# Performance work log

Measured on AMD Instinct MI355X. Metric: run time of the kernel, lower is better.

Reference implementation:

```python
import jax, jax.numpy as jnp
import numpy as np

MEMORY_SIZE = 40
INPUT_SIZE = 256
OUTPUT_SIZE = 256
BATCH = 16
SEQ = 4096


def setup_inputs() -> dict:
    key = jax.random.key(0)
    k1, k2, k3, k4 = jax.random.split(key, 4)
    x = jax.random.normal(k1, (BATCH, SEQ, INPUT_SIZE), dtype=jnp.float32)
    # xavier-uniform-style init for params
    lim_w = float(np.sqrt(6.0 / (INPUT_SIZE + OUTPUT_SIZE)))
    W1 = jax.random.uniform(k2, (INPUT_SIZE, OUTPUT_SIZE), minval=-lim_w, maxval=lim_w, dtype=jnp.float32)
    W2 = jax.random.uniform(k3, (INPUT_SIZE, OUTPUT_SIZE), minval=-lim_w, maxval=lim_w, dtype=jnp.float32)
    bias = jnp.ones((OUTPUT_SIZE,), dtype=jnp.float32)
    lim_m = float(np.sqrt(6.0 / (MEMORY_SIZE + 1 + INPUT_SIZE)))
    mw = jax.random.uniform(k4, (MEMORY_SIZE + 1, INPUT_SIZE), minval=-lim_m, maxval=lim_m, dtype=jnp.float32)
    mw = mw.at[0].set(0.0)  # torch init zeros row 0 (it stays trainable though)
    return {"input_data": x, "W1": W1, "W2": W2, "bias": bias, "memory_weights": mw}


def reference(input_data, W1, W2, bias, memory_weights):
    # Faithful to: idx(i,j) = i-j if 1 <= i-j <= memory_size else 0;
    # h_hatt[b,i,d] = sum_j memory_weights[idx(i,j), d] * x[b,j,d]
    # = sum_{l=1..m} w[l]*x[i-l]  +  w[0]*(sum_j x[j] - window sum).
    m = memory_weights.shape[0] - 1
    B, T, D = input_data.shape
    total = jnp.sum(input_data, axis=1, keepdims=True)  # [B,1,D]
    h_hatt = jnp.zeros_like(input_data)
    win = jnp.zeros_like(input_data)
    for l in range(1, m + 1):  # fixed small memory order
        shifted = jnp.pad(input_data[:, : T - l], ((0, 0), (l, 0), (0, 0)))
        h_hatt = h_hatt + memory_weights[l] * shifted
        win = win + shifted
    h_hatt = h_hatt + memory_weights[0] * (total - win)
    return input_data @ W1 + h_hatt @ W2 + bias
```

## Files before the change

kernel.cpp:

```cpp
#include <hip/hip_runtime.h>
#include <hip/hip_bf16.h>
#include <stdint.h>

#define NBATCH 16
#define SEQ 4096
#define DIM 256
#define MEM 40
#define KTOT 512
#define MTOT (NBATCH*SEQ)

typedef unsigned short u16;
typedef __attribute__((ext_vector_type(8))) short short8;
typedef __attribute__((ext_vector_type(4))) float f32x4;

typedef __attribute__((address_space(1))) const void gvoid_t;
typedef __attribute__((address_space(3))) void lvoid_t;

static __device__ __forceinline__ u16 f2bf(float f) {
    union { float f; uint32_t u; } v; v.f = f;
    uint32_t u = v.u;
    u += 0x7FFFu + ((u >> 16) & 1);
    return (u16)(u >> 16);
}

__global__ __launch_bounds__(256) void k_bmat(const float* __restrict__ W1,
                                              const float* __restrict__ W2,
                                              uint32_t* __restrict__ BmT32) {
    const int n = blockIdx.x;
    const int d = threadIdx.x;
    float w1 = W1[d * DIM + n];
    float w2 = W2[d * DIM + n];
    BmT32[n * DIM + d] = (uint32_t)f2bf(w1) | ((uint32_t)f2bf(w2) << 16);
}

#define TCHUNK 128
__global__ __launch_bounds__(256) void k_conv(const float* __restrict__ x,
                                              const float* __restrict__ mw,
                                              uint32_t* __restrict__ Aout,
                                              float* __restrict__ total) {
    const int d = threadIdx.x;
    const int b = blockIdx.y;
    const int t0 = blockIdx.x * TCHUNK;

    const float mw0 = mw[d];
    float wp[MEM];
#pragma unroll
    for (int l = 0; l < MEM; ++l) wp[l] = mw[(l + 1) * DIM + d] - mw0;

    const float* xb = x + (size_t)b * SEQ * DIM;
    uint32_t* Ab = Aout + (size_t)b * SEQ * DIM;

    float hist[MEM];
#pragma unroll
    for (int j = 0; j < MEM; ++j) {
        int t = t0 - MEM + j;
        hist[j] = (t >= 0) ? xb[(size_t)t * DIM + d] : 0.0f;
    }

    float colsum = 0.0f;
    for (int s = 0; s < TCHUNK / 8; ++s) {
        const int t = t0 + s * 8;
        float cur[8];
#pragma unroll
        for (int i = 0; i < 8; ++i) cur[i] = xb[(size_t)(t + i) * DIM + d];
#pragma unroll
        for (int i = 0; i < 8; ++i) colsum += cur[i];

        float h[8];
#pragma unroll
        for (int i = 0; i < 8; ++i) {
            float acc = 0.0f;
#pragma unroll
            for (int l = 1; l <= MEM; ++l) {
                float v = (i - l >= 0) ? cur[i - l] : hist[MEM + i - l];
                acc += wp[l - 1] * v;
            }
            h[i] = acc;
        }
#pragma unroll
        for (int i = 0; i < 8; ++i) {
            uint32_t pack = (uint32_t)f2bf(cur[i]) | ((uint32_t)f2bf(h[i]) << 16);
            Ab[(size_t)(t + i) * DIM + d] = pack;
        }
#pragma unroll
        for (int j = 0; j < MEM - 8; ++j) hist[j] = hist[j + 8];
#pragma unroll
        for (int i = 0; i < 8; ++i) hist[MEM - 8 + i] = cur[i];
    }
    atomicAdd(&total[b * DIM + d], colsum);
}

__global__ __launch_bounds__(256) void k_corr(const float* __restrict__ W2,
                                              const float* __restrict__ bias,
                                              const float* __restrict__ mw,
                                              const float* __restrict__ total,
                                              float* __restrict__ corr) {
    const int b = blockIdx.x;
    const int n = threadIdx.x;
    float s = bias[n];
    for (int dd = 0; dd < DIM; ++dd)
        s += mw[dd] * total[b * DIM + dd] * W2[dd * DIM + n];
    corr[b * DIM + n] = s;
}

#define BM 128
#define BN 256
#define BK 64

__global__ __launch_bounds__(512) void k_gemm(const u16* A,
                                              const u16* __restrict__ BmT,
                                              const float* __restrict__ corr,
                                              float* out) {
    __shared__ __align__(16) u16 Alds[BM * BK];
    __shared__ __align__(16) u16 Blds[BN * BK];

    const int tid  = threadIdx.x;
    const int lane = tid & 63;
    const int w    = tid >> 6;
    const int wr   = w >> 2;
    const int wc   = w & 3;
    const int m0   = blockIdx.x * BM;

    f32x4 acc[4][4] = {};

    for (int kt = 0; kt < KTOT / BK; ++kt) {
        const int k0 = kt * BK;
#pragma unroll
        for (int i = 0; i < 2; ++i) {
            int c   = i * 512 + tid;
            int row = c >> 3;
            int kin = (c & 7) * 8;
            const u16* g = A + ((size_t)(m0 + row) * KTOT + k0 + kin);
            char* l = (char*)Alds + (size_t)(i * 512 + (tid & ~63)) * 16;
            __builtin_amdgcn_global_load_lds((gvoid_t*)g, (lvoid_t*)l, 16, 0, 0);
        }
#pragma unroll
        for (int i = 0; i < 4; ++i) {
            int c   = i * 512 + tid;
            int n   = c >> 3;
            int kin = (c & 7) * 8;
            const u16* g = BmT + ((size_t)n * KTOT + k0 + kin);
            char* l = (char*)Blds + (size_t)(i * 512 + (tid & ~63)) * 16;
            __builtin_amdgcn_global_load_lds((gvoid_t*)g, (lvoid_t*)l, 16, 0, 0);
        }
        __syncthreads();

#pragma unroll
        for (int kk = 0; kk < 2; ++kk) {
            short8 af[4], bfr[4];
#pragma unroll
            for (int mi = 0; mi < 4; ++mi) {
                int r = wr * 64 + mi * 16 + (lane & 15);
                af[mi] = *(const short8*)(Alds + r * BK + kk * 32 + ((lane >> 4) * 8));
            }
#pragma unroll
            for (int ni = 0; ni < 4; ++ni) {
                int ccol = wc * 64 + ni * 16 + (lane & 15);
                bfr[ni] = *(const short8*)(Blds + ccol * BK + kk * 32 + ((lane >> 4) * 8));
            }
#pragma unroll
            for (int mi = 0; mi < 4; ++mi)
#pragma unroll
                for (int ni = 0; ni < 4; ++ni)
                    acc[mi][ni] = __builtin_amdgcn_mfma_f32_16x16x32_bf16(
                        af[mi], bfr[ni], acc[mi][ni], 0, 0, 0);
        }
        __syncthreads();
    }

    const int bidx = m0 >> 12;
    const float* corr_b = corr + bidx * DIM;
#pragma unroll
    for (int ni = 0; ni < 4; ++ni) {
        int col = wc * 64 + ni * 16 + (lane & 15);
        float cv = corr_b[col];
#pragma unroll
        for (int mi = 0; mi < 4; ++mi) {
            int rbase = m0 + wr * 64 + mi * 16 + ((lane >> 4) * 4);
#pragma unroll
            for (int j = 0; j < 4; ++j)
                out[(size_t)(rbase + j) * DIM + col] = acc[mi][ni][j] + cv;
        }
    }
}

extern "C" void kernel_launch(void* const* d_in, const int* in_sizes, int n_in,
                              void* d_out, int out_size, void* d_ws, size_t ws_size,
                              hipStream_t stream) {
    const float* x    = (const float*)d_in[0];
    const float* W1   = (const float*)d_in[1];
    const float* W2   = (const float*)d_in[2];
    const float* bias = (const float*)d_in[3];
    const float* mw   = (const float*)d_in[4];
    float* out = (float*)d_out;

    u16*   BmT   = (u16*)d_ws;
    float* total = (float*)((char*)d_ws + 262144);
    float* corr  = (float*)((char*)d_ws + 262144 + 16384);

    hipMemsetAsync(total, 0, NBATCH * DIM * sizeof(float), stream);
    k_bmat<<<dim3(DIM), dim3(256), 0, stream>>>(W1, W2, (uint32_t*)BmT);
    k_conv<<<dim3(SEQ / TCHUNK, NBATCH), dim3(256), 0, stream>>>(
        x, mw, (uint32_t*)d_out, total);
    k_corr<<<dim3(NBATCH), dim3(256), 0, stream>>>(W2, bias, mw, total, corr);
    k_gemm<<<dim3(MTOT / BM), dim3(512), 0, stream>>>(
        (const u16*)d_out, BmT, corr, out);
}
```

Baseline: 80.59 us.

## Split conv taps across four lanes per channel with shuffle reduction

The causal conv kernel now gives each channel four lanes, each handling 10 of the 40 taps. The lead lane loads fresh inputs and hands older samples to its neighbours through shuffles, and partial sums are combined with xor shuffles. The grid grows by four along a new z dimension, which cuts per-thread registers and serial FMA work and raises occupancy. In exchange it adds shuffle traffic and idles three of four lanes during stores. Loads are now 16 channels wide (64B segments), which may hurt coalescing.

New measurement: 98.09 us. 21.7% more time.

```diff
diff --git a/kernel.cpp b/kernel.cpp
--- a/kernel.cpp
+++ b/kernel.cpp
@@ -38,56 +38,64 @@
                                               const float* __restrict__ mw,
                                               uint32_t* __restrict__ Aout,
                                               float* __restrict__ total) {
-    const int d = threadIdx.x;
-    const int b = blockIdx.y;
-    const int t0 = blockIdx.x * TCHUNK;
+    const int tid  = threadIdx.x;
+    const int lane = tid & 63;
+    const int wid  = tid >> 6;
+    const int c    = lane & 15;
+    const int s    = lane >> 4;
+    const int d    = blockIdx.z * 64 + wid * 16 + c;
+    const int b    = blockIdx.y;
+    const int t0   = blockIdx.x * TCHUNK;
+    const bool lead = (s == 0);
+
+    const float* xb = x + (size_t)b * SEQ * DIM + d;
+    uint32_t* Ab = Aout + (size_t)b * SEQ * DIM + d;
 
     const float mw0 = mw[d];
-    float wp[MEM];
-#pragma unroll
-    for (int l = 0; l < MEM; ++l) wp[l] = mw[(l + 1) * DIM + d] - mw0;
-
-    const float* xb = x + (size_t)b * SEQ * DIM;
-    uint32_t* Ab = Aout + (size_t)b * SEQ * DIM;
-
-    float hist[MEM];
-#pragma unroll
-    for (int j = 0; j < MEM; ++j) {
-        int t = t0 - MEM + j;
-        hist[j] = (t >= 0) ? xb[(size_t)t * DIM + d] : 0.0f;
+    float wp[10];
+#pragma unroll
+    for (int j = 0; j < 10; ++j)
+        wp[j] = mw[(10 * s + 1 + j) * DIM + d] - mw0;
+
+    float S[10];
+#pragma unroll
+    for (int m = 0; m < 10; ++m) {
+        int t = t0 - 10 * s - 10 + m;
+        S[m] = (t >= 0) ? xb[(size_t)t * DIM] : 0.0f;
     }
 
     float colsum = 0.0f;
-    for (int s = 0; s < TCHUNK / 8; ++s) {
-        const int t = t0 + s * 8;
-        float cur[8];
-#pragma unroll
-        for (int i = 0; i < 8; ++i) cur[i] = xb[(size_t)(t + i) * DIM + d];
-#pragma unroll
-        for (int i = 0; i < 8; ++i) colsum += cur[i];
-
-        float h[8];
-#pragma unroll
-        for (int i = 0; i < 8; ++i) {
-            float acc = 0.0f;
-#pragma unroll
-            for (int l = 1; l <= MEM; ++l) {
-                float v = (i - l >= 0) ? cur[i - l] : hist[MEM + i - l];
-                acc += wp[l - 1] * v;
-            }
-            h[i] = acc;
-        }
-#pragma unroll
-        for (int i = 0; i < 8; ++i) {
-            uint32_t pack = (uint32_t)f2bf(cur[i]) | ((uint32_t)f2bf(h[i]) << 16);
-            Ab[(size_t)(t + i) * DIM + d] = pack;
-        }
-#pragma unroll
-        for (int j = 0; j < MEM - 8; ++j) hist[j] = hist[j + 8];
-#pragma unroll
-        for (int i = 0; i < 8; ++i) hist[MEM - 8 + i] = cur[i];
-    }
-    atomicAdd(&total[b * DIM + d], colsum);
+    for (int it = 0; it < TCHUNK / 16; ++it) {
+        const int tb = t0 + it * 16;
+        float I[16];
+#pragma unroll
+        for (int i = 0; i < 16; ++i) {
+            float fresh = xb[(size_t)(tb + i) * DIM];
+            float donor = (i < 10) ? S[i] : I[i - 10];
+            float passed = __shfl_up(donor, 16, 64);
+            I[i] = lead ? fresh : passed;
+        }
+#pragma unroll
+        for (int i = 0; i < 16; ++i) {
+            float h = 0.0f;
+#pragma unroll
+            for (int j = 0; j < 10; ++j) {
+                int m = i + 9 - j;
+                float v = (m < 10) ? S[m] : I[m - 10];
+                h = fmaf(wp[j], v, h);
+            }
+            h += __shfl_xor(h, 16, 64);
+            h += __shfl_xor(h, 32, 64);
+            colsum += I[i];
+            if (lead) {
+                __hip_bfloat162 p = __float22bfloat162_rn(make_float2(I[i], h));
+                Ab[(size_t)(tb + i) * DIM] = *reinterpret_cast<uint32_t*>(&p);
+            }
+        }
+#pragma unroll
+        for (int k = 0; k < 10; ++k) S[k] = I[6 + k];
+    }
+    if (lead) atomicAdd(&total[b * DIM + d], colsum);
 }
 
 __global__ __launch_bounds__(256) void k_corr(const float* __restrict__ W2,
@@ -200,7 +208,7 @@
 
     hipMemsetAsync(total, 0, NBATCH * DIM * sizeof(float), stream);
     k_bmat<<<dim3(DIM), dim3(256), 0, stream>>>(W1, W2, (uint32_t*)BmT);
-    k_conv<<<dim3(SEQ / TCHUNK, NBATCH), dim3(256), 0, stream>>>(
+    k_conv<<<dim3(SEQ / TCHUNK, NBATCH, DIM / 64), dim3(256), 0, stream>>>(
         x, mw, (uint32_t*)d_out, total);
     k_corr<<<dim3(NBATCH), dim3(256), 0, stream>>>(W2, bias, mw, total, corr);
     k_gemm<<<dim3(MTOT / BM), dim3(512), 0, stream>>>(
```

## Restructure conv kernel to stream window loads with smaller time chunks

Applied to the files above, without the earlier changes.

The causal convolution kernel no longer keeps a shifting 40-entry register history. Each group of 4 outputs now re-reads its 44-row input window from global memory (cache-served) and accumulates 4 outputs with FMAs as values stream in. Time chunks shrink from 128 to 32, giving 4x more blocks for parallelism. A guard-free template path is used when the window does not touch t<0, and sched_barriers limit register pressure. The cost is about 11x redundant global/L2 reads per output row in exchange for fewer registers and higher occupancy.

Measured after the change: 169.2 us. 2.1x slower.

```diff
diff --git a/kernel.cpp b/kernel.cpp
--- a/kernel.cpp
+++ b/kernel.cpp
@@ -33,60 +33,74 @@
     BmT32[n * DIM + d] = (uint32_t)f2bf(w1) | ((uint32_t)f2bf(w2) << 16);
 }
 
-#define TCHUNK 128
-__global__ __launch_bounds__(256) void k_conv(const float* __restrict__ x,
-                                              const float* __restrict__ mw,
-                                              uint32_t* __restrict__ Aout,
-                                              float* __restrict__ total) {
-    const int d = threadIdx.x;
-    const int b = blockIdx.y;
-    const int t0 = blockIdx.x * TCHUNK;
+#define TC 32
+
+template <bool GUARD>
+__device__ __forceinline__ void conv_body(const float* __restrict__ xb,
+                                          uint32_t* __restrict__ Ab,
+                                          const float (&wp)[MEM],
+                                          int t0, float& colsum) {
+    for (int it = 0; it < TC / 4; ++it) {
+        const int tb = t0 + it * 4;
+        const float* bp = xb + (size_t)(tb - MEM) * DIM;
+        float h0 = 0.f, h1 = 0.f, h2 = 0.f, h3 = 0.f;
+        float c0 = 0.f, c1 = 0.f, c2 = 0.f, c3 = 0.f;
+#pragma unroll
+        for (int j = 0; j <= MEM + 3; ++j) {
+            float v;
+            if (GUARD) {
+                int m = tb - MEM + j;
+                int mc = m < 0 ? 0 : m;
+                v = xb[(size_t)mc * DIM];
+                v = m < 0 ? 0.f : v;
+            } else {
+                v = bp[(size_t)j * DIM];
+            }
+            const int moff = j - MEM;
+            if (moff == 0) c0 = v;
+            if (moff == 1) c1 = v;
+            if (moff == 2) c2 = v;
+            if (moff == 3) c3 = v;
+            { int l = 0 - moff; if (l >= 1 && l <= MEM) h0 = fmaf(wp[l - 1], v, h0); }
+            { int l = 1 - moff; if (l >= 1 && l <= MEM) h1 = fmaf(wp[l - 1], v, h1); }
+            { int l = 2 - moff; if (l >= 1 && l <= MEM) h2 = fmaf(wp[l - 1], v, h2); }
+            { int l = 3 - moff; if (l >= 1 && l <= MEM) h3 = fmaf(wp[l - 1], v, h3); }
+            if ((j % 11) == 10) __builtin_amdgcn_sched_barrier(0);
+        }
+        colsum += c0 + c1 + c2 + c3;
+        __hip_bfloat162 p0 = __float22bfloat162_rn(make_float2(c0, h0));
+        __hip_bfloat162 p1 = __float22bfloat162_rn(make_float2(c1, h1));
+        __hip_bfloat162 p2 = __float22bfloat162_rn(make_float2(c2, h2));
+        __hip_bfloat162 p3 = __float22bfloat162_rn(make_float2(c3, h3));
+        Ab[(size_t)(tb + 0) * DIM] = *reinterpret_cast<uint32_t*>(&p0);
+        Ab[(size_t)(tb + 1) * DIM] = *reinterpret_cast<uint32_t*>(&p1);
+        Ab[(size_t)(tb + 2) * DIM] = *reinterpret_cast<uint32_t*>(&p2);
+        Ab[(size_t)(tb + 3) * DIM] = *reinterpret_cast<uint32_t*>(&p3);
+    }
+}
+
+__global__ void k_conv(const float* __restrict__ x,
+                       const float* __restrict__ mw,
+                       uint32_t* __restrict__ Aout,
+                       float* __restrict__ total) {
+    const int d  = threadIdx.x;
+    const int b  = blockIdx.y;
+    const int t0 = blockIdx.x * TC;
 
     const float mw0 = mw[d];
     float wp[MEM];
 #pragma unroll
     for (int l = 0; l < MEM; ++l) wp[l] = mw[(l + 1) * DIM + d] - mw0;
 
-    const float* xb = x + (size_t)b * SEQ * DIM;
-    uint32_t* Ab = Aout + (size_t)b * SEQ * DIM;
-
-    float hist[MEM];
-#pragma unroll
-    for (int j = 0; j < MEM; ++j) {
-        int t = t0 - MEM + j;
-        hist[j] = (t >= 0) ? xb[(size_t)t * DIM + d] : 0.0f;
-    }
+    const float* xb = x + (size_t)b * SEQ * DIM + d;
+    uint32_t* Ab    = Aout + (size_t)b * SEQ * DIM + d;
 
     float colsum = 0.0f;
-    for (int s = 0; s < TCHUNK / 8; ++s) {
-        const int t = t0 + s * 8;
-        float cur[8];
-#pragma unroll
-        for (int i = 0; i < 8; ++i) cur[i] = xb[(size_t)(t + i) * DIM + d];
-#pragma unroll
-        for (int i = 0; i < 8; ++i) colsum += cur[i];
-
-        float h[8];
-#pragma unroll
-        for (int i = 0; i < 8; ++i) {
-            float acc = 0.0f;
-#pragma unroll
-            for (int l = 1; l <= MEM; ++l) {
-                float v = (i - l >= 0) ? cur[i - l] : hist[MEM + i - l];
-                acc += wp[l - 1] * v;
-            }
-            h[i] = acc;
-        }
-#pragma unroll
-        for (int i = 0; i < 8; ++i) {
-            uint32_t pack = (uint32_t)f2bf(cur[i]) | ((uint32_t)f2bf(h[i]) << 16);
-            Ab[(size_t)(t + i) * DIM + d] = pack;
-        }
-#pragma unroll
-        for (int j = 0; j < MEM - 8; ++j) hist[j] = hist[j + 8];
-#pragma unroll
-        for (int i = 0; i < 8; ++i) hist[MEM - 8 + i] = cur[i];
-    }
+    if (t0 >= MEM)
+        conv_body<false>(xb, Ab, wp, t0, colsum);
+    else
+        conv_body<true>(xb, Ab, wp, t0, colsum);
+
     atomicAdd(&total[b * DIM + d], colsum);
 }
 
@@ -200,7 +214,7 @@
 
     hipMemsetAsync(total, 0, NBATCH * DIM * sizeof(float), stream);
     k_bmat<<<dim3(DIM), dim3(256), 0, stream>>>(W1, W2, (uint32_t*)BmT);
-    k_conv<<<dim3(SEQ / TCHUNK, NBATCH), dim3(256), 0, stream>>>(
+    k_conv<<<dim3(SEQ / TC, NBATCH), dim3(256), 0, stream>>>(
         x, mw, (uint32_t*)d_out, total);
     k_corr<<<dim3(NBATCH), dim3(256), 0, stream>>>(W2, bias, mw, total, corr);
     k_gemm<<<dim3(MTOT / BM), dim3(512), 0, stream>>>(
```

## Split conv taps across half-waves, shrink time chunks, and swizzle GEMM block order

Applied to the files above, without the earlier changes.

The convolution kernel now splits the 40 memory taps between the two 32-lane halves of each wavefront, with 20 taps per half. It combines the partial sums with a cross-lane shuffle, uses 64-step time chunks, and adds a z-dimension over channel halves. This cuts per-thread register pressure and serial FMA depth and launches more blocks for better occupancy. The cost is duplicated loads of x and half the lanes sitting idle during stores. The GEMM block index is also remapped with a bid&7 interleave, which changes the order rows are processed and may affect cache or channel locality.

Result: slower. 94.45 us (+17.2%).

```diff
diff --git a/kernel.cpp b/kernel.cpp
--- a/kernel.cpp
+++ b/kernel.cpp
@@ -33,61 +33,93 @@
     BmT32[n * DIM + d] = (uint32_t)f2bf(w1) | ((uint32_t)f2bf(w2) << 16);
 }
 
-#define TCHUNK 128
-__global__ __launch_bounds__(256) void k_conv(const float* __restrict__ x,
-                                              const float* __restrict__ mw,
-                                              uint32_t* __restrict__ Aout,
-                                              float* __restrict__ total) {
-    const int d = threadIdx.x;
-    const int b = blockIdx.y;
-    const int t0 = blockIdx.x * TCHUNK;
-
+#define TW 64
+
+template <bool GUARD>
+__device__ __forceinline__ void conv_wave(const float* __restrict__ xb,
+                                          uint32_t* __restrict__ Ab,
+                                          const float* __restrict__ mw,
+                                          float* __restrict__ total,
+                                          int d, int b, int t0, int g, bool lead) {
     const float mw0 = mw[d];
-    float wp[MEM];
-#pragma unroll
-    for (int l = 0; l < MEM; ++l) wp[l] = mw[(l + 1) * DIM + d] - mw0;
-
-    const float* xb = x + (size_t)b * SEQ * DIM;
-    uint32_t* Ab = Aout + (size_t)b * SEQ * DIM;
-
-    float hist[MEM];
-#pragma unroll
-    for (int j = 0; j < MEM; ++j) {
-        int t = t0 - MEM + j;
-        hist[j] = (t >= 0) ? xb[(size_t)t * DIM + d] : 0.0f;
+    float wt[20];
+#pragma unroll
+    for (int j = 0; j < 20; ++j)
+        wt[j] = mw[(20 * g + j + 1) * DIM + d] - mw0;
+
+    const int tg = t0 - 20 * g;
+    float hist[20];
+#pragma unroll
+    for (int m = 0; m < 20; ++m) {
+        int t = tg - 20 + m;
+        if (GUARD)
+            hist[m] = (t >= 0) ? xb[(size_t)t * DIM] : 0.0f;
+        else
+            hist[m] = xb[(size_t)t * DIM];
     }
 
     float colsum = 0.0f;
-    for (int s = 0; s < TCHUNK / 8; ++s) {
-        const int t = t0 + s * 8;
-        float cur[8];
-#pragma unroll
-        for (int i = 0; i < 8; ++i) cur[i] = xb[(size_t)(t + i) * DIM + d];
-#pragma unroll
-        for (int i = 0; i < 8; ++i) colsum += cur[i];
-
-        float h[8];
-#pragma unroll
-        for (int i = 0; i < 8; ++i) {
+#pragma unroll
+    for (int ch = 0; ch < TW / 4; ++ch) {
+        const int tb = tg + ch * 4;
+        float cur[4];
+#pragma unroll
+        for (int i = 0; i < 4; ++i) {
+            int tt = tb + i;
+            if (GUARD)
+                cur[i] = (tt >= 0) ? xb[(size_t)tt * DIM] : 0.0f;
+            else
+                cur[i] = xb[(size_t)tt * DIM];
+        }
+        float h[4];
+#pragma unroll
+        for (int i = 0; i < 4; ++i) {
             float acc = 0.0f;
 #pragma unroll
-            for (int l = 1; l <= MEM; ++l) {
-                float v = (i - l >= 0) ? cur[i - l] : hist[MEM + i - l];
-                acc += wp[l - 1] * v;
+            for (int j = 0; j < 20; ++j) {
+                int m = i + 19 - j;
+                float v = (m < 20) ? hist[m] : cur[m - 20];
+                acc = fmaf(wt[j], v, acc);
             }
             h[i] = acc;
         }
 #pragma unroll
-        for (int i = 0; i < 8; ++i) {
-            uint32_t pack = (uint32_t)f2bf(cur[i]) | ((uint32_t)f2bf(h[i]) << 16);
-            Ab[(size_t)(t + i) * DIM + d] = pack;
-        }
-#pragma unroll
-        for (int j = 0; j < MEM - 8; ++j) hist[j] = hist[j + 8];
-#pragma unroll
-        for (int i = 0; i < 8; ++i) hist[MEM - 8 + i] = cur[i];
-    }
-    atomicAdd(&total[b * DIM + d], colsum);
+        for (int i = 0; i < 4; ++i) {
+            float hs = h[i] + __shfl_xor(h[i], 32, 64);
+            if (lead) {
+                colsum += cur[i];
+                __hip_bfloat162 p = __float22bfloat162_rn(make_float2(cur[i], hs));
+                Ab[(size_t)(t0 + ch * 4 + i) * DIM] = *reinterpret_cast<uint32_t*>(&p);
+            }
+        }
+#pragma unroll
+        for (int m = 0; m < 16; ++m) hist[m] = hist[m + 4];
+#pragma unroll
+        for (int i = 0; i < 4; ++i) hist[16 + i] = cur[i];
+    }
+    if (lead) atomicAdd(&total[b * DIM + d], colsum);
+}
+
+__global__ void k_conv(const float* __restrict__ x,
+                       const float* __restrict__ mw,
+                       uint32_t* __restrict__ Aout,
+                       float* __restrict__ total) {
+    const int tid  = threadIdx.x;
+    const int lane = tid & 63;
+    const int w    = tid >> 6;
+    const int c    = lane & 31;
+    const int g    = lane >> 5;
+    const int d    = blockIdx.z * 128 + w * 32 + c;
+    const int b    = blockIdx.y;
+    const int t0   = blockIdx.x * TW;
+
+    const float* xb = x + (size_t)b * SEQ * DIM + d;
+    uint32_t* Ab    = Aout + (size_t)b * SEQ * DIM + d;
+
+    if (blockIdx.x == 0)
+        conv_wave<true >(xb, Ab, mw, total, d, b, t0, g, g == 0);
+    else
+        conv_wave<false>(xb, Ab, mw, total, d, b, t0, g, g == 0);
 }
 
 __global__ __launch_bounds__(256) void k_corr(const float* __restrict__ W2,
@@ -119,7 +151,9 @@
     const int w    = tid >> 6;
     const int wr   = w >> 2;
     const int wc   = w & 3;
-    const int m0   = blockIdx.x * BM;
+    const int bid  = blockIdx.x;
+    const int swz  = (bid & 7) * 64 + (bid >> 3);
+    const int m0   = swz * BM;
 
     f32x4 acc[4][4] = {};
 
@@ -200,7 +234,7 @@
 
     hipMemsetAsync(total, 0, NBATCH * DIM * sizeof(float), stream);
     k_bmat<<<dim3(DIM), dim3(256), 0, stream>>>(W1, W2, (uint32_t*)BmT);
-    k_conv<<<dim3(SEQ / TCHUNK, NBATCH), dim3(256), 0, stream>>>(
+    k_conv<<<dim3(SEQ / TW, NBATCH, 2), dim3(256), 0, stream>>>(
         x, mw, (uint32_t*)d_out, total);
     k_corr<<<dim3(NBATCH), dim3(256), 0, stream>>>(W2, bias, mw, total, corr);
     k_gemm<<<dim3(MTOT / BM), dim3(512), 0, stream>>>(
```
